# Kernel optimization log

Measured on AMD Instinct MI355X. Metric: run time of the kernel, lower is better.

Reference implementation:

```python
import jax, jax.numpy as jnp
import numpy as np

B, H, NSTEPS = 4096, 1024, 10
T0, T1 = 0.0, 1.0


def setup_inputs() -> dict:
    key = jax.random.key(0)
    k0, k1, k2, k3 = jax.random.split(key, 4)
    s = 0.03  # keep tanh in active region
    return {
        "h0": jax.random.normal(k0, (B, H), dtype=jnp.float32),
        "W1": jax.random.normal(k1, (H + 1, 2 * H), dtype=jnp.float32) * s,
        "b1": jnp.zeros((2 * H,), dtype=jnp.float32),
        "W2": jax.random.normal(k2, (2 * H, 2 * H), dtype=jnp.float32) * s,
        "b2": jnp.zeros((2 * H,), dtype=jnp.float32),
        "W3": jax.random.normal(k3, (2 * H, H), dtype=jnp.float32) * s,
        "b3": jnp.zeros((H,), dtype=jnp.float32),
    }


def _ode_func(t, h, W1, b1, W2, b2, W3, b3):
    # time-dependent: append a column of t to the state  -> (B, H+1)
    tcol = jnp.full((h.shape[0], 1), t, dtype=h.dtype)
    x = jnp.concatenate([h, tcol], axis=1)
    x = jnp.tanh(x @ W1 + b1)
    x = jnp.tanh(x @ W2 + b2)
    return x @ W3 + b3  # (B, H)


def _integrate(h0, W1, b1, W2, b2, W3, b3):
    t = jnp.linspace(T0, T1, NSTEPS + 1, dtype=jnp.float32)
    dt = t[1:] - t[:-1]

    def f(ti, h):
        return _ode_func(ti, h, W1, b1, W2, b2, W3, b3)

    def step(h, td):
        ti, dti = td
        k1 = f(ti, h)
        k2 = f(ti + dti / 2, h + (dti / 2) * k1)
        k3 = f(ti + dti / 2, h + (dti / 2) * k2)
        k4 = f(ti + dti, h + dti * k3)
        h_next = h + (dti / 6) * (k1 + 2 * k2 + 2 * k3 + k4)
        return h_next, None

    h1, _ = jax.lax.scan(step, h0, (t[:-1], dt))
    return h1


def reference(h0, W1, b1, W2, b2, W3, b3):
    return _integrate(h0, W1, b1, W2, b2, W3, b3)
```

## Files before the change

kernel.cpp:

```cpp
#include <hip/hip_runtime.h>
#include <cstdint>
#include <cstddef>

typedef _Float16 half8 __attribute__((ext_vector_type(8)));
typedef float floatx4 __attribute__((ext_vector_type(4)));

typedef __attribute__((address_space(3))) unsigned lds_u32;
typedef const __attribute__((address_space(1))) unsigned glb_u32;

#define BK 64

__device__ __forceinline__ void glds16(const void* g, void* l) {
    __builtin_amdgcn_global_load_lds((glb_u32*)g, (lds_u32*)l, 16, 0, 0);
}

__device__ __forceinline__ float fast_tanh(float x) {
    float ax = fabsf(x);
    float e  = __expf(-2.0f * ax);
    float t  = (1.0f - e) / (1.0f + e);
    return x < 0.0f ? -t : t;
}

template <int MT, int NT, int NPX>
__device__ __forceinline__ void map_block(int id, int& mt, int& nt) {
    constexpr int NG  = NT / NPX;
    constexpr int XPG = 8 / NG;
    const int xcd  = id & 7;
    const int slot = id >> 3;
    nt = (xcd % NG) * NPX + (slot % NPX);
    mt = (xcd / NG) * (MT / XPG) + slot / NPX;
}

template <int TBM, int TBN, int MF, int NF, int NW>
__device__ __forceinline__ void gemm_acc_db(const _Float16* __restrict__ A,
                                            const _Float16* __restrict__ BT,
                                            unsigned m0, unsigned n0,
                                            int K, floatx4 acc[MF][NF]) {
    constexpr int CW = TBN / (16 * NF);
    constexpr int RW = TBM / (16 * MF);
    static_assert(RW * CW == NW, "wave grid must use all waves");
    constexpr int AH  = TBM * 32;
    constexpr int BH  = TBN * 32;
    constexpr int NCA = TBM / 16;
    constexpr int NCB = TBN / 16;
    constexpr int UA  = (NCA + NW - 1) / NW;
    constexpr int UB  = (NCB + NW - 1) / NW;

    __shared__ __align__(16) _Float16 As[2][TBM * BK];
    __shared__ __align__(16) _Float16 Bs[2][TBN * BK];

    const int tid  = threadIdx.x;
    const int lane = tid & 63;
    const int wid  = tid >> 6;

    const int srow = lane >> 2;
    const int skq  = (lane & 3) ^ ((lane >> 3) & 3);
    const int quad = lane >> 4;
    const int l16  = lane & 15;
    const int wm   = (wid / CW) * (16 * MF);
    const int wn   = (wid % CW) * (16 * NF);

    const unsigned kstr = (unsigned)K * 2u;
    const unsigned aB0  = (m0 + (unsigned)srow) * kstr + (unsigned)(skq * 16);
    const unsigned bB0  = (n0 + (unsigned)srow) * kstr + (unsigned)(skq * 16);
    const char* Abase = (const char*)A;
    const char* Bbase = (const char*)BT;

#pragma unroll
    for (int i = 0; i < MF; ++i)
#pragma unroll
        for (int j = 0; j < NF; ++j)
            acc[i][j] = 0.0f;

    auto stage = [&](int buf, unsigned kb) {
#pragma unroll
        for (int h = 0; h < 2; ++h) {
#pragma unroll
            for (int u = 0; u < UA; ++u) {
                const int c = wid + u * NW;
                if ((NCA % NW == 0) || c < NCA)
                    glds16(Abase + (aB0 + (unsigned)c * (16u * kstr) + kb + (unsigned)(h * 64)),
                           &As[buf][h * AH + c * 512]);
            }
#pragma unroll
            for (int u = 0; u < UB; ++u) {
                const int c = wid + u * NW;
                if ((NCB % NW == 0) || c < NCB)
                    glds16(Bbase + (bB0 + (unsigned)c * (16u * kstr) + kb + (unsigned)(h * 64)),
                           &Bs[buf][h * BH + c * 512]);
            }
        }
    };

    const int rdoff = l16 * 32 + ((quad ^ ((l16 >> 1) & 3)) << 3);
    const unsigned Kb = (unsigned)K * 2u;
    const unsigned BKb = BK * 2u;

    stage(0, 0);
    int cur = 0;
    for (unsigned kb = 0; kb < Kb; kb += BKb) {
        __syncthreads();
        if (kb + BKb < Kb) stage(cur ^ 1, kb + BKb);

#pragma unroll
        for (int h = 0; h < 2; ++h) {
            half8 av[MF], bv[NF];
#pragma unroll
            for (int i = 0; i < MF; ++i)
                av[i] = *(const half8*)(&As[cur][h * AH + ((wm >> 4) + i) * 512 + rdoff]);
#pragma unroll
            for (int j = 0; j < NF; ++j)
                bv[j] = *(const half8*)(&Bs[cur][h * BH + ((wn >> 4) + j) * 512 + rdoff]);
#pragma unroll
            for (int i = 0; i < MF; ++i)
#pragma unroll
                for (int j = 0; j < NF; ++j)
                    acc[i][j] = __builtin_amdgcn_mfma_f32_16x16x32_f16(av[i], bv[j], acc[i][j], 0, 0, 0);
        }
        cur ^= 1;
    }
}


template <bool WITH_T, int MT, int NT>
__global__ __launch_bounds__(512)
void gemm_bias_tanh(const _Float16* __restrict__ A, const _Float16* __restrict__ BT,
                    _Float16* __restrict__ out, const float* __restrict__ bias,
                    const float* __restrict__ brow, float t, int N, int K) {
    int mt, nt;
    map_block<MT, NT, 4>(blockIdx.x, mt, nt);
    const unsigned bm0 = (unsigned)mt * 128;
    const unsigned bn0 = (unsigned)nt * 128;

    floatx4 acc[4][2];
    gemm_acc_db<128, 128, 4, 2, 8>(A, BT, bm0, bn0, K, acc);

    const int tid  = threadIdx.x;
    const int lane = tid & 63;
    const int wid  = tid >> 6;
    const int quad = lane >> 4;
    const int l16  = lane & 15;
    const size_t m0 = bm0 + (size_t)(wid / 4) * 64;
    const size_t n0 = bn0 + (size_t)(wid % 4) * 32;

#pragma unroll
    for (int j = 0; j < 2; ++j) {
        const size_t col = n0 + j * 16 + l16;
        float b = bias[col];
        if (WITH_T) b += t * brow[col];
#pragma unroll
        for (int i = 0; i < 4; ++i) {
            const size_t rbase = m0 + i * 16 + quad * 4;
#pragma unroll
            for (int r = 0; r < 4; ++r) {
                out[(rbase + r) * (size_t)N + col] = (_Float16)fast_tanh(acc[i][j][r] + b);
            }
        }
    }
}

__global__ __launch_bounds__(512)
void gemm_k_stage(const _Float16* __restrict__ A, const _Float16* __restrict__ BT,
                  const float* __restrict__ bias, float* __restrict__ hstate,
                  float* __restrict__ accb, _Float16* __restrict__ x,
                  int stage, float c, float dt6, int N, int K) {
    int mt, nt;
    map_block<64, 8, 2>(blockIdx.x, mt, nt);
    const unsigned bm0 = (unsigned)mt * 64;
    const unsigned bn0 = (unsigned)nt * 128;

    floatx4 acc[2][2];
    gemm_acc_db<64, 128, 2, 2, 8>(A, BT, bm0, bn0, K, acc);

    const int tid  = threadIdx.x;
    const int lane = tid & 63;
    const int wid  = tid >> 6;
    const int quad = lane >> 4;
    const int l16  = lane & 15;
    const size_t m0 = bm0 + (size_t)(wid / 4) * 32;
    const size_t n0 = bn0 + (size_t)(wid % 4) * 32;

#pragma unroll
    for (int j = 0; j < 2; ++j) {
        const size_t col = n0 + j * 16 + l16;
        const float b = bias[col];
#pragma unroll
        for (int i = 0; i < 2; ++i) {
            const size_t rbase = m0 + i * 16 + quad * 4;
#pragma unroll
            for (int r = 0; r < 4; ++r) {
                const size_t idx = (rbase + r) * (size_t)N + col;
                const float k = acc[i][j][r] + b;
                if (stage == 0) {
                    accb[idx] = k;
                    x[idx] = (_Float16)(hstate[idx] + c * k);
                } else if (stage < 3) {
                    accb[idx] += 2.0f * k;
                    x[idx] = (_Float16)(hstate[idx] + c * k);
                } else {
                    const float hn = hstate[idx] + dt6 * (accb[idx] + k);
                    hstate[idx] = hn;
                    x[idx] = (_Float16)hn;
                }
            }
        }
    }
}

__global__ __launch_bounds__(256)
void transposeW(const float* __restrict__ W, _Float16* __restrict__ WT,
                int K, int N) {
    __shared__ float tile[32][33];
    const int tx = threadIdx.x;
    const int ty = threadIdx.y;
    const int n0 = blockIdx.x * 32;
    const int k0 = blockIdx.y * 32;
#pragma unroll
    for (int r = ty; r < 32; r += 8)
        tile[r][tx] = W[(size_t)(k0 + r) * N + n0 + tx];
    __syncthreads();
#pragma unroll
    for (int r = ty; r < 32; r += 8)
        WT[(size_t)(n0 + r) * K + k0 + tx] = (_Float16)tile[tx][r];
}

__global__ void copy_row(const float* __restrict__ W1, float* __restrict__ w1row, int N) {
    const int n = blockIdx.x * 256 + threadIdx.x;
    if (n < N) w1row[n] = W1[(size_t)1024 * N + n];
}

__global__ void init_h(const float* __restrict__ h0, float* __restrict__ hstate,
                       _Float16* __restrict__ x, int n) {
    const int i = blockIdx.x * 256 + threadIdx.x;
    if (i < n) {
        const float v = h0[i];
        hstate[i] = v;
        x[i] = (_Float16)v;
    }
}

extern "C" void kernel_launch(void* const* d_in, const int* in_sizes, int n_in,
                              void* d_out, int out_size, void* d_ws, size_t ws_size,
                              hipStream_t stream) {
    const int B = 4096, H = 1024, H2 = 2048;

    const float* h0 = (const float*)d_in[0];
    const float* W1 = (const float*)d_in[1];
    const float* b1 = (const float*)d_in[2];
    const float* W2 = (const float*)d_in[3];
    const float* b2 = (const float*)d_in[4];
    const float* W3 = (const float*)d_in[5];
    const float* b3 = (const float*)d_in[6];

    float* hstate = (float*)d_out;

    char* ws = (char*)d_ws;
    _Float16* x    = (_Float16*)ws; ws += (size_t)B * H  * 2;
    _Float16* a1   = (_Float16*)ws; ws += (size_t)B * H2 * 2;
    _Float16* a2   = (_Float16*)ws; ws += (size_t)B * H2 * 2;
    float*    accb = (float*)ws;    ws += (size_t)B * H  * 4;
    _Float16* W1T  = (_Float16*)ws; ws += (size_t)H2 * H  * 2;
    _Float16* W2T  = (_Float16*)ws; ws += (size_t)H2 * H2 * 2;
    _Float16* W3T  = (_Float16*)ws; ws += (size_t)H  * H2 * 2;
    float*   w1row = (float*)ws;    ws += (size_t)H2 * 4;

    const dim3 tblk(32, 8);
    transposeW<<<dim3(H2 / 32, H  / 32), tblk, 0, stream>>>(W1, W1T, H,  H2);
    transposeW<<<dim3(H2 / 32, H2 / 32), tblk, 0, stream>>>(W2, W2T, H2, H2);
    transposeW<<<dim3(H  / 32, H2 / 32), tblk, 0, stream>>>(W3, W3T, H2, H);
    copy_row<<<dim3(H2 / 256), 256, 0, stream>>>(W1, w1row, H2);
    init_h<<<dim3((B * H + 255) / 256), 256, 0, stream>>>(h0, hstate, x, B * H);

    const float dt  = 0.1f;
    const float dt2 = 0.05f;
    const float dt6 = dt / 6.0f;

    const dim3 blk(512);
    const int g12 = (B / 128) * (H2 / 128);
    const int g3  = (B / 64) * (H / 128);

    for (int s = 0; s < 10; ++s) {
        const float ti = (float)s * dt;

        gemm_bias_tanh<true , 32, 16><<<g12, blk, 0, stream>>>(x,  W1T, a1, b1, w1row, ti,       H2, H);
        gemm_bias_tanh<false, 32, 16><<<g12, blk, 0, stream>>>(a1, W2T, a2, b2, nullptr, 0.f,    H2, H2);
        gemm_k_stage<<<g3, blk, 0, stream>>>(a2, W3T, b3, hstate, accb, x, 0, dt2, dt6, H, H2);

        gemm_bias_tanh<true , 32, 16><<<g12, blk, 0, stream>>>(x,  W1T, a1, b1, w1row, ti + dt2, H2, H);
        gemm_bias_tanh<false, 32, 16><<<g12, blk, 0, stream>>>(a1, W2T, a2, b2, nullptr, 0.f,    H2, H2);
        gemm_k_stage<<<g3, blk, 0, stream>>>(a2, W3T, b3, hstate, accb, x, 1, dt2, dt6, H, H2);

        gemm_bias_tanh<true , 32, 16><<<g12, blk, 0, stream>>>(x,  W1T, a1, b1, w1row, ti + dt2, H2, H);
        gemm_bias_tanh<false, 32, 16><<<g12, blk, 0, stream>>>(a1, W2T, a2, b2, nullptr, 0.f,    H2, H2);
        gemm_k_stage<<<g3, blk, 0, stream>>>(a2, W3T, b3, hstate, accb, x, 2, dt,  dt6, H, H2);

        gemm_bias_tanh<true , 32, 16><<<g12, blk, 0, stream>>>(x,  W1T, a1, b1, w1row, ti + dt,  H2, H);
        gemm_bias_tanh<false, 32, 16><<<g12, blk, 0, stream>>>(a1, W2T, a2, b2, nullptr, 0.f,    H2, H2);
        gemm_k_stage<<<g3, blk, 0, stream>>>(a2, W3T, b3, hstate, accb, x, 3, dt,  dt6, H, H2);
    }
}
```

Baseline: 4.247 ms.

## Use single-buffered 256-thread GEMM with 4x4 wave tiles for tanh layers

Replaces the double-buffered 512-thread GEMM mainloop in the two tanh layers with a single-buffered 256-thread version. Each wave now computes a 64x64 sub-tile (4x4 MFMA fragments) instead of 64x32. LDS per block is halved and launch bounds ask for 3 blocks per CU, so occupancy should cover latency in place of explicit prefetch. The cost is no overlap of the global-to-LDS copy with compute inside a block, an extra barrier per K step, and higher register pressure from 16 accumulators.

```diff
diff --git a/kernel.cpp b/kernel.cpp
--- a/kernel.cpp
+++ b/kernel.cpp
@@ -29,6 +29,82 @@
     const int slot = id >> 3;
     nt = (xcd % NG) * NPX + (slot % NPX);
     mt = (xcd / NG) * (MT / XPG) + slot / NPX;
+}
+
+
+template <int MF, int NF>
+__device__ __forceinline__ void gemm_acc_sb128(const _Float16* __restrict__ A,
+                                               const _Float16* __restrict__ BT,
+                                               unsigned m0, unsigned n0,
+                                               int K, floatx4 acc[MF][NF]) {
+    constexpr int AH = 128 * 32;
+    constexpr int BH = 128 * 32;
+
+    __shared__ __align__(16) _Float16 As[128 * BK];
+    __shared__ __align__(16) _Float16 Bs[128 * BK];
+
+    const int tid  = threadIdx.x;
+    const int lane = tid & 63;
+    const int wid  = tid >> 6;
+
+    const int srow = lane >> 2;
+    const int skq  = (lane & 3) ^ ((lane >> 3) & 3);
+    const int quad = lane >> 4;
+    const int l16  = lane & 15;
+    const int wmc  = (wid >> 1) * 4;
+    const int wnc  = (wid & 1) * 4;
+    const int rdoff = l16 * 32 + ((quad ^ ((l16 >> 1) & 3)) << 3);
+
+    const unsigned kstr = (unsigned)K * 2u;
+    const unsigned aB0  = (m0 + (unsigned)srow) * kstr + (unsigned)(skq * 16);
+    const unsigned bB0  = (n0 + (unsigned)srow) * kstr + (unsigned)(skq * 16);
+    const char* Abase = (const char*)A;
+    const char* Bbase = (const char*)BT;
+
+#pragma unroll
+    for (int i = 0; i < MF; ++i)
+#pragma unroll
+        for (int j = 0; j < NF; ++j)
+            acc[i][j] = 0.0f;
+
+    const unsigned Kb  = (unsigned)K * 2u;
+    const unsigned BKb = BK * 2u;
+
+    for (unsigned kb = 0; kb < Kb; kb += BKb) {
+#pragma unroll
+        for (int h = 0; h < 2; ++h) {
+#pragma unroll
+            for (int u = 0; u < 2; ++u) {
+                const int c = wid + u * 4;
+                glds16(Abase + (aB0 + (unsigned)c * (16u * kstr) + kb + (unsigned)(h * 64)),
+                       &As[h * AH + c * 512]);
+            }
+#pragma unroll
+            for (int u = 0; u < 2; ++u) {
+                const int c = wid + u * 4;
+                glds16(Bbase + (bB0 + (unsigned)c * (16u * kstr) + kb + (unsigned)(h * 64)),
+                       &Bs[h * BH + c * 512]);
+            }
+        }
+        __syncthreads();
+
+#pragma unroll
+        for (int h = 0; h < 2; ++h) {
+            half8 av[MF], bv[NF];
+#pragma unroll
+            for (int i = 0; i < MF; ++i)
+                av[i] = *(const half8*)(&As[h * AH + (wmc + i) * 512 + rdoff]);
+#pragma unroll
+            for (int j = 0; j < NF; ++j)
+                bv[j] = *(const half8*)(&Bs[h * BH + (wnc + j) * 512 + rdoff]);
+#pragma unroll
+            for (int i = 0; i < MF; ++i)
+#pragma unroll
+                for (int j = 0; j < NF; ++j)
+                    acc[i][j] = __builtin_amdgcn_mfma_f32_16x16x32_f16(av[i], bv[j], acc[i][j], 0, 0, 0);
+        }
+        __syncthreads();
+    }
 }
 
 template <int TBM, int TBN, int MF, int NF, int NW>
@@ -93,7 +169,7 @@
     };
 
     const int rdoff = l16 * 32 + ((quad ^ ((l16 >> 1) & 3)) << 3);
-    const unsigned Kb = (unsigned)K * 2u;
+    const unsigned Kb  = (unsigned)K * 2u;
     const unsigned BKb = BK * 2u;
 
     stage(0, 0);
@@ -123,7 +199,7 @@
 
 
 template <bool WITH_T, int MT, int NT>
-__global__ __launch_bounds__(512)
+__global__ __launch_bounds__(256, 3)
 void gemm_bias_tanh(const _Float16* __restrict__ A, const _Float16* __restrict__ BT,
                     _Float16* __restrict__ out, const float* __restrict__ bias,
                     const float* __restrict__ brow, float t, int N, int K) {
@@ -132,19 +208,19 @@
     const unsigned bm0 = (unsigned)mt * 128;
     const unsigned bn0 = (unsigned)nt * 128;
 
-    floatx4 acc[4][2];
-    gemm_acc_db<128, 128, 4, 2, 8>(A, BT, bm0, bn0, K, acc);
+    floatx4 acc[4][4];
+    gemm_acc_sb128<4, 4>(A, BT, bm0, bn0, K, acc);
 
     const int tid  = threadIdx.x;
     const int lane = tid & 63;
     const int wid  = tid >> 6;
     const int quad = lane >> 4;
     const int l16  = lane & 15;
-    const size_t m0 = bm0 + (size_t)(wid / 4) * 64;
-    const size_t n0 = bn0 + (size_t)(wid % 4) * 32;
-
-#pragma unroll
-    for (int j = 0; j < 2; ++j) {
+    const size_t m0 = bm0 + (size_t)(wid >> 1) * 64;
+    const size_t n0 = bn0 + (size_t)(wid & 1) * 64;
+
+#pragma unroll
+    for (int j = 0; j < 4; ++j) {
         const size_t col = n0 + j * 16 + l16;
         float b = bias[col];
         if (WITH_T) b += t * brow[col];
@@ -275,27 +351,28 @@
     const float dt2 = 0.05f;
     const float dt6 = dt / 6.0f;
 
-    const dim3 blk(512);
+    const dim3 blk12(256);
+    const dim3 blk3(512);
     const int g12 = (B / 128) * (H2 / 128);
     const int g3  = (B / 64) * (H / 128);
 
     for (int s = 0; s < 10; ++s) {
         const float ti = (float)s * dt;
 
-        gemm_bias_tanh<true , 32, 16><<<g12, blk, 0, stream>>>(x,  W1T, a1, b1, w1row, ti,       H2, H);
-        gemm_bias_tanh<false, 32, 16><<<g12, blk, 0, stream>>>(a1, W2T, a2, b2, nullptr, 0.f,    H2, H2);
-        gemm_k_stage<<<g3, blk, 0, stream>>>(a2, W3T, b3, hstate, accb, x, 0, dt2, dt6, H, H2);
-
-        gemm_bias_tanh<true , 32, 16><<<g12, blk, 0, stream>>>(x,  W1T, a1, b1, w1row, ti + dt2, H2, H);
-        gemm_bias_tanh<false, 32, 16><<<g12, blk, 0, stream>>>(a1, W2T, a2, b2, nullptr, 0.f,    H2, H2);
-        gemm_k_stage<<<g3, blk, 0, stream>>>(a2, W3T, b3, hstate, accb, x, 1, dt2, dt6, H, H2);
-
-        gemm_bias_tanh<true , 32, 16><<<g12, blk, 0, stream>>>(x,  W1T, a1, b1, w1row, ti + dt2, H2, H);
-        gemm_bias_tanh<false, 32, 16><<<g12, blk, 0, stream>>>(a1, W2T, a2, b2, nullptr, 0.f,    H2, H2);
-        gemm_k_stage<<<g3, blk, 0, stream>>>(a2, W3T, b3, hstate, accb, x, 2, dt,  dt6, H, H2);
-
-        gemm_bias_tanh<true , 32, 16><<<g12, blk, 0, stream>>>(x,  W1T, a1, b1, w1row, ti + dt,  H2, H);
-        gemm_bias_tanh<false, 32, 16><<<g12, blk, 0, stream>>>(a1, W2T, a2, b2, nullptr, 0.f,    H2, H2);
-        gemm_k_stage<<<g3, blk, 0, stream>>>(a2, W3T, b3, hstate, accb, x, 3, dt,  dt6, H, H2);
-    }
-}
+        gemm_bias_tanh<true , 32, 16><<<g12, blk12, 0, stream>>>(x,  W1T, a1, b1, w1row, ti,       H2, H);
+        gemm_bias_tanh<false, 32, 16><<<g12, blk12, 0, stream>>>(a1, W2T, a2, b2, nullptr, 0.f,    H2, H2);
+        gemm_k_stage<<<g3, blk3, 0, stream>>>(a2, W3T, b3, hstate, accb, x, 0, dt2, dt6, H, H2);
+
+        gemm_bias_tanh<true , 32, 16><<<g12, blk12, 0, stream>>>(x,  W1T, a1, b1, w1row, ti + dt2, H2, H);
+        gemm_bias_tanh<false, 32, 16><<<g12, blk12, 0, stream>>>(a1, W2T, a2, b2, nullptr, 0.f,    H2, H2);
+        gemm_k_stage<<<g3, blk3, 0, stream>>>(a2, W3T, b3, hstate, accb, x, 1, dt2, dt6, H, H2);
+
+        gemm_bias_tanh<true , 32, 16><<<g12, blk12, 0, stream>>>(x,  W1T, a1, b1, w1row, ti + dt2, H2, H);
+        gemm_bias_tanh<false, 32, 16><<<g12, blk12, 0, stream>>>(a1, W2T, a2, b2, nullptr, 0.f,    H2, H2);
+        gemm_k_stage<<<g3, blk3, 0, stream>>>(a2, W3T, b3, hstate, accb, x, 2, dt,  dt6, H, H2);
+
+        gemm_bias_tanh<true , 32, 16><<<g12, blk12, 0, stream>>>(x,  W1T, a1, b1, w1row, ti + dt,  H2, H);
+        gemm_bias_tanh<false, 32, 16><<<g12, blk12, 0, stream>>>(a1, W2T, a2, b2, nullptr, 0.f,    H2, H2);
+        gemm_k_stage<<<g3, blk3, 0, stream>>>(a2, W3T, b3, hstate, accb, x, 3, dt,  dt6, H, H2);
+    }
+}
```

New measurement: 4.335 ms. 1.02x slower.
